# Performance work log

Hardware: AMD Instinct MI355X
Metric: run time of the kernel (lower is better)

## Reference

```python
import jax, jax.numpy as jnp
import numpy as np

PAD_IDX = 0
H = 500  # hidden_size hardcoded in the module
V = 50000
E = 500


def gru_scan(xs, h0, Wih, Whh, bih, bhh):
    """PyTorch-convention GRU over sequence. xs: (S, in), h0: (H,)."""
    def step(h, x):
        gi = x @ Wih.T + bih          # (3H,)
        gh = h @ Whh.T + bhh          # (3H,)
        ir, iz, inn = jnp.split(gi, 3)
        hr, hz, hn = jnp.split(gh, 3)
        r = jax.nn.sigmoid(ir + hr)
        z = jax.nn.sigmoid(iz + hz)
        n = jnp.tanh(inn + r * hn)
        h_new = (1.0 - z) * n + z * h
        return h_new, h_new
    h_last, hs = jax.lax.scan(step, h0, xs)
    return hs, h_last


def setup_inputs() -> dict:
    key = jax.random.key(0)
    ks = jax.random.split(key, 16)
    s = 0.05
    inp = {
        "encoder_input": jax.random.randint(ks[0], (512,), 0, V),
        "target_tensor": jax.random.randint(ks[1], (512,), 0, V),
        "encoder_hidden": jnp.zeros((1, 1, H), jnp.float32),
        # encoder params
        "enc_emb": jax.random.normal(ks[2], (V, E), jnp.float32) * s,
        "enc_Wih": jax.random.normal(ks[3], (3 * H, E), jnp.float32) * s,
        "enc_Whh": jax.random.normal(ks[4], (3 * H, H), jnp.float32) * s,
        "enc_bih": jax.random.normal(ks[5], (3 * H,), jnp.float32) * s,
        "enc_bhh": jax.random.normal(ks[6], (3 * H,), jnp.float32) * s,
        # decoder params
        "dec_emb": jax.random.normal(ks[7], (V, H), jnp.float32) * s,
        "dec_Wih": jax.random.normal(ks[8], (3 * H, H), jnp.float32) * s,
        "dec_Whh": jax.random.normal(ks[9], (3 * H, H), jnp.float32) * s,
        "dec_bih": jax.random.normal(ks[10], (3 * H,), jnp.float32) * s,
        "dec_bhh": jax.random.normal(ks[11], (3 * H,), jnp.float32) * s,
        "out_W": jax.random.normal(ks[12], (V, H), jnp.float32) * s,
        "out_b": jax.random.normal(ks[13], (V,), jnp.float32) * s,
    }
    return inp


def reference(encoder_input, target_tensor, encoder_hidden,
              enc_emb, enc_Wih, enc_Whh, enc_bih, enc_bhh,
              dec_emb, dec_Wih, dec_Whh, dec_bih, dec_bhh,
              out_W, out_b):
    # ---- Encoder: per-token GRU loop == one GRU scan over the sequence ----
    enc_x = enc_emb[encoder_input]                       # (S, E); dropout is identity (p=0 / eval)
    h0 = encoder_hidden[0, 0]                            # (H,)
    _, enc_h = gru_scan(enc_x, h0, enc_Wih, enc_Whh, enc_bih, enc_bhh)

    # ---- Decoder: teacher forcing; input di is target[di-1], first is PAD ----
    dec_in = jnp.concatenate([jnp.array([PAD_IDX], encoder_input.dtype),
                              target_tensor[:-1]])       # (T,)
    dec_x = jax.nn.relu(dec_emb[dec_in])                 # (T, H)
    dec_hs, _ = gru_scan(dec_x, enc_h, dec_Wih, dec_Whh, dec_bih, dec_bhh)  # (T, H)

    logits = dec_hs @ out_W.T + out_b                    # (T, V)
    logp = jax.nn.log_softmax(logits, axis=1)
    T = target_tensor.shape[0]
    # NLLLoss per step (batch=1 -> mean == single value), summed over steps
    loss = -jnp.sum(logp[jnp.arange(T), target_tensor])
    decoder_outputs = jnp.argmax(logp, axis=1).astype(jnp.int64)
    return loss, enc_h.reshape(1, 1, H), decoder_outputs
```

## Files before the change

kernel.cpp:

```cpp
#include <hip/hip_runtime.h>
#include <cstdint>
#include <cstddef>

#define H    500
#define G3   1500
#define SEQ  512
#define V    50000
#define NT   391

#define NB   25
#define HSL  20
#define ROWS 60

static constexpr size_t OFS_HBUF_E = 0;
static constexpr size_t OFS_HBUF_D = 16384;
static constexpr size_t OFS_ENCH   = 32768;
static constexpr size_t OFS_GI_ENC = 65536;
static constexpr size_t OFS_GI_DEC = OFS_GI_ENC + 3276800;
static constexpr size_t OFS_DECHS  = OFS_GI_DEC + 3276800;
static constexpr size_t OFS_SPART  = OFS_DECHS + 1048576;
static constexpr size_t OFS_PPART  = OFS_SPART + 1048576;
static constexpr size_t OFS_LTGT   = OFS_PPART + 2097152;
static constexpr size_t OFS_SFIN   = OFS_LTGT + 4096;

#define GI_BM 64
#define GI_BN 64
#define GI_BK 20
__global__ __launch_bounds__(256) void k_gi_gemm(
    const float* __restrict__ eA, const float* __restrict__ WA,
    const float* __restrict__ bA, const int* __restrict__ tA,
    const float* __restrict__ eB, const float* __restrict__ WB,
    const float* __restrict__ bB, const int* __restrict__ tB,
    float* __restrict__ GiA, float* __restrict__ GiB)
{
    const int dec = blockIdx.z;
    const float* emb = dec ? eB : eA;
    const float* Wih = dec ? WB : WA;
    const float* bih = dec ? bB : bA;
    const int*  toks = dec ? tB : tA;
    float* Gi        = dec ? GiB : GiA;

    __shared__ __align__(16) float As[GI_BK * GI_BM];
    __shared__ __align__(16) float Bs[GI_BK * GI_BN];
    const int tid = threadIdx.x;
    const int n0 = blockIdx.x * GI_BN;
    const int m0 = blockIdx.y * GI_BM;
    const int tx = tid & 15, ty = tid >> 4;
    float acc[4][4] = {};
    for (int k0 = 0; k0 < H; k0 += GI_BK) {
        for (int x = tid; x < 320; x += 256) {
            int m = x / 5, kq = x - m * 5;
            int gm = m0 + m;
            int tok = dec ? ((gm == 0) ? 0 : toks[gm - 1]) : toks[gm];
            float4 v = *(const float4*)(emb + (size_t)tok * H + k0 + kq * 4);
            if (dec) { v.x = fmaxf(v.x, 0.f); v.y = fmaxf(v.y, 0.f);
                       v.z = fmaxf(v.z, 0.f); v.w = fmaxf(v.w, 0.f); }
            int kb = kq * 4;
            As[(kb + 0) * GI_BM + m] = v.x; As[(kb + 1) * GI_BM + m] = v.y;
            As[(kb + 2) * GI_BM + m] = v.z; As[(kb + 3) * GI_BM + m] = v.w;
        }
        for (int x = tid; x < 320; x += 256) {
            int n = x / 5, kq = x - n * 5;
            int gn = n0 + n;
            float4 v = make_float4(0.f, 0.f, 0.f, 0.f);
            if (gn < G3) v = *(const float4*)(Wih + (size_t)gn * H + k0 + kq * 4);
            int kb = kq * 4;
            Bs[(kb + 0) * GI_BN + n] = v.x; Bs[(kb + 1) * GI_BN + n] = v.y;
            Bs[(kb + 2) * GI_BN + n] = v.z; Bs[(kb + 3) * GI_BN + n] = v.w;
        }
        __syncthreads();
#pragma unroll 5
        for (int kk = 0; kk < GI_BK; ++kk) {
            float a[4], b[4];
            *(float4*)&a[0] = *(const float4*)&As[kk * GI_BM + ty * 4];
            *(float4*)&b[0] = *(const float4*)&Bs[kk * GI_BN + tx * 4];
#pragma unroll
            for (int i = 0; i < 4; i++)
#pragma unroll
                for (int j = 0; j < 4; j++) acc[i][j] = fmaf(a[i], b[j], acc[i][j]);
        }
        __syncthreads();
    }
#pragma unroll
    for (int i = 0; i < 4; i++) {
        int gm = m0 + ty * 4 + i;
#pragma unroll
        for (int j = 0; j < 4; j++) {
            int gn = n0 + tx * 4 + j;
            if (gn < G3) Gi[(size_t)gm * G3 + gn] = acc[i][j] + bih[gn];
        }
    }
}

__global__ __launch_bounds__(256, 1) void k_gru(
    const float* __restrict__ Whh, const float* __restrict__ bhh,
    const float* __restrict__ Gi, const float* __restrict__ h0,
    unsigned long long* hbuf, float* hfinal, float* hs_out, float* douth, int S)
{
    __shared__ __align__(16) float h_s[H];
    __shared__ float p_s[ROWS * 26];
    __shared__ float gh_s[ROWS];
    const int tid = threadIdx.x;
    const int wg = blockIdx.x;
    const int j0 = wg * HSL;

    const int g = tid / 25;
    const int s = tid - g * 25;
    const int slc = tid / 10;
    const int e0  = 2 * (tid - slc * 10);

    float wreg[6][20];
    if (tid < 250) {
#pragma unroll
        for (int r = 0; r < 6; ++r) {
            const int rl = g * 6 + r;
            const int gate = rl / 20, jl = rl - gate * 20;
            const float* wr = Whh + (size_t)(gate * 500 + j0 + jl) * H + s * 20;
#pragma unroll
            for (int c = 0; c < 5; ++c)
                *(float4*)&wreg[r][c * 4] = *(const float4*)(wr + c * 4);
        }
    }
    float bb = 0.f;
    if (tid < ROWS) {
        const int gate = tid / 20, jl = tid - gate * 20;
        bb = bhh[gate * 500 + j0 + jl];
    }
    float hown = (tid < HSL) ? h0[j0 + tid] : 0.f;

    if (tid < HSL)
        __hip_atomic_store(hbuf + 800 + wg * 32 + tid,
                           ((unsigned long long)1u << 32) | (unsigned)__float_as_uint(hown),
                           __ATOMIC_RELAXED, __HIP_MEMORY_SCOPE_AGENT);

    for (int t = 0; t < S; ++t) {
        const unsigned want = (unsigned)(t + 1);
        const int rb = (t + 1) & 1;
        float ir = 0.f, iz = 0.f, inn = 0.f;
        if (tid < HSL) {
            const float* gi = Gi + (size_t)t * G3 + j0 + tid;
            ir = gi[0]; iz = gi[500]; inn = gi[1000];
        }
        if (tid < 250) {
            const unsigned long long* pa = hbuf + rb * 800 + slc * 32 + e0;
            unsigned long long v0, v1;
            do {
                v0 = __hip_atomic_load(pa,     __ATOMIC_RELAXED, __HIP_MEMORY_SCOPE_AGENT);
                v1 = __hip_atomic_load(pa + 1, __ATOMIC_RELAXED, __HIP_MEMORY_SCOPE_AGENT);
            } while (((unsigned)(v0 >> 32) != want) || ((unsigned)(v1 >> 32) != want));
            h_s[2 * tid]     = __uint_as_float((unsigned)v0);
            h_s[2 * tid + 1] = __uint_as_float((unsigned)v1);
        }
        __syncthreads();
        if (tid < 250) {
            float hv[20];
#pragma unroll
            for (int c = 0; c < 5; ++c)
                *(float4*)&hv[c * 4] = *(const float4*)&h_s[s * 20 + c * 4];
            float acc[6] = {0.f, 0.f, 0.f, 0.f, 0.f, 0.f};
#pragma unroll
            for (int i = 0; i < 20; ++i)
#pragma unroll
                for (int r = 0; r < 6; ++r) acc[r] = fmaf(wreg[r][i], hv[i], acc[r]);
#pragma unroll
            for (int r = 0; r < 6; ++r) p_s[(g * 6 + r) * 26 + s] = acc[r];
        }
        __syncthreads();
        if (tid < ROWS) {
            float sum = 0.f;
#pragma unroll 5
            for (int i = 0; i < 25; ++i) sum += p_s[tid * 26 + i];
            gh_s[tid] = sum + bb;
        }
        __syncthreads();
        if (tid < HSL) {
            const int j = j0 + tid;
            const float hr = gh_s[tid], hz = gh_s[HSL + tid], hn = gh_s[2 * HSL + tid];
            const float r = 1.f / (1.f + __expf(-(ir + hr)));
            const float z = 1.f / (1.f + __expf(-(iz + hz)));
            const float n = tanhf(inn + r * hn);
            const float hnew = (1.f - z) * n + z * hown;
            hown = hnew;
            __hip_atomic_store(hbuf + (t & 1) * 800 + wg * 32 + tid,
                               ((unsigned long long)(unsigned)(t + 2) << 32) |
                               (unsigned)__float_as_uint(hnew),
                               __ATOMIC_RELAXED, __HIP_MEMORY_SCOPE_AGENT);
            if (hs_out) hs_out[(size_t)t * H + j] = hnew;
            if (t == S - 1) {
                if (hfinal) hfinal[j] = hnew;
                if (douth)  douth[j]  = hnew;
            }
        }
    }
}

#define LG_BM 128
#define LG_BN 128
#define LG_BK 20
__global__ __launch_bounds__(256) void k_logits(
    const float* __restrict__ A, const float* __restrict__ Bw,
    const float* __restrict__ bias,
    float* __restrict__ S_part, unsigned long long* __restrict__ P_part)
{
    __shared__ __align__(16) float As[LG_BK * LG_BM];
    __shared__ __align__(16) float Bs[LG_BK * LG_BN];
    const int tid = threadIdx.x;
    const int bx = blockIdx.x;
    const int n0 = bx * LG_BN;
    const int m0 = blockIdx.y * LG_BM;
    const int tx = tid & 15, ty = tid >> 4;
    float acc[8][8] = {};
    for (int k0 = 0; k0 < H; k0 += LG_BK) {
        for (int x = tid; x < LG_BM * LG_BK; x += 256) {
            int m = x / LG_BK, k = x - m * LG_BK;
            As[k * LG_BM + m] = A[(size_t)(m0 + m) * H + k0 + k];
        }
        for (int x = tid; x < LG_BN * LG_BK; x += 256) {
            int n = x / LG_BK, k = x - n * LG_BK;
            int gn = n0 + n;
            Bs[k * LG_BN + n] = (gn < V) ? Bw[(size_t)gn * H + k0 + k] : 0.f;
        }
        __syncthreads();
#pragma unroll 5
        for (int kk = 0; kk < LG_BK; ++kk) {
            float a[8], b[8];
            *(float4*)&a[0] = *(const float4*)&As[kk * LG_BM + ty * 8];
            *(float4*)&a[4] = *(const float4*)&As[kk * LG_BM + ty * 8 + 4];
            *(float4*)&b[0] = *(const float4*)&Bs[kk * LG_BN + tx * 8];
            *(float4*)&b[4] = *(const float4*)&Bs[kk * LG_BN + tx * 8 + 4];
#pragma unroll
            for (int i = 0; i < 8; i++)
#pragma unroll
                for (int j = 0; j < 8; j++) acc[i][j] = fmaf(a[i], b[j], acc[i][j]);
        }
        __syncthreads();
    }
    float bcol[8]; int gncol[8]; bool bval[8];
#pragma unroll
    for (int j = 0; j < 8; j++) {
        int gn = n0 + tx * 8 + j;
        gncol[j] = gn; bval[j] = gn < V; bcol[j] = bval[j] ? bias[gn] : 0.f;
    }
#pragma unroll
    for (int i = 0; i < 8; i++) {
        int gm = m0 + ty * 8 + i;
        float mx = -3.4e38f; unsigned mi = 0; float se = 0.f;
#pragma unroll
        for (int j = 0; j < 8; j++) {
            if (bval[j]) {
                float l = acc[i][j] + bcol[j];
                se += __expf(l);
                if (l > mx) { mx = l; mi = (unsigned)gncol[j]; }
            }
        }
        unsigned u = __float_as_uint(mx);
        unsigned key = (u & 0x80000000u) ? ~u : (u | 0x80000000u);
        unsigned long long pk = ((unsigned long long)key << 32) |
                                (unsigned long long)(0xFFFFFFFFu - mi);
#pragma unroll
        for (int off = 1; off < 16; off <<= 1) {
            unsigned long long pk2 = __shfl_xor(pk, off);
            se += __shfl_xor(se, off);
            if (pk2 > pk) pk = pk2;
        }
        if (tx == 0) {
            S_part[(size_t)gm * NT + bx] = se;
            P_part[(size_t)gm * NT + bx] = pk;
        }
    }
}

__global__ __launch_bounds__(128) void k_reduce_rows(
    const float* __restrict__ S_part, const unsigned long long* __restrict__ P_part,
    float* __restrict__ Sfin, float* __restrict__ out_argmax)
{
    const int row = blockIdx.x, tid = threadIdx.x;
    float s = 0.f; unsigned long long p = 0ull;
    for (int i = tid; i < NT; i += 128) {
        s += S_part[(size_t)row * NT + i];
        unsigned long long q = P_part[(size_t)row * NT + i];
        if (q > p) p = q;
    }
#pragma unroll
    for (int off = 1; off < 64; off <<= 1) {
        s += __shfl_xor(s, off);
        unsigned long long q = __shfl_xor(p, off);
        if (q > p) p = q;
    }
    __shared__ float s2[2];
    __shared__ unsigned long long p2[2];
    if ((tid & 63) == 0) { s2[tid >> 6] = s; p2[tid >> 6] = p; }
    __syncthreads();
    if (tid == 0) {
        s = s2[0] + s2[1];
        p = p2[0] > p2[1] ? p2[0] : p2[1];
        Sfin[row] = s;
        unsigned idx = 0xFFFFFFFFu - (unsigned)(p & 0xFFFFFFFFull);
        out_argmax[row] = (float)idx;
    }
}

__global__ __launch_bounds__(64) void k_ltgt(
    const float* __restrict__ A, const float* __restrict__ Bw,
    const float* __restrict__ bias, const int* __restrict__ tgt,
    float* __restrict__ ltgt)
{
    const int row = blockIdx.x, lane = threadIdx.x;
    const int tok = tgt[row];
    const float* a = A + (size_t)row * H;
    const float* b = Bw + (size_t)tok * H;
    float s = 0.f;
    for (int k = lane; k < H; k += 64) s = fmaf(a[k], b[k], s);
#pragma unroll
    for (int off = 1; off < 64; off <<= 1) s += __shfl_xor(s, off);
    if (lane == 0) ltgt[row] = s + bias[tok];
}

__global__ __launch_bounds__(512) void k_final(
    const float* __restrict__ Sfin, const float* __restrict__ ltgt, float* __restrict__ d_out)
{
    __shared__ float red[512];
    const int t = threadIdx.x;
    red[t] = logf(Sfin[t]) - ltgt[t];
    __syncthreads();
    for (int s = 256; s > 0; s >>= 1) {
        if (t < s) red[t] += red[t + s];
        __syncthreads();
    }
    if (t == 0) d_out[0] = red[0];
}

extern "C" void kernel_launch(void* const* d_in, const int* in_sizes, int n_in,
                              void* d_out, int out_size, void* d_ws, size_t ws_size,
                              hipStream_t stream) {
    const int*   enc_ids = (const int*)d_in[0];
    const int*   tgt     = (const int*)d_in[1];
    const float* enc_h0  = (const float*)d_in[2];
    const float* enc_emb = (const float*)d_in[3];
    const float* enc_Wih = (const float*)d_in[4];
    const float* enc_Whh = (const float*)d_in[5];
    const float* enc_bih = (const float*)d_in[6];
    const float* enc_bhh = (const float*)d_in[7];
    const float* dec_emb = (const float*)d_in[8];
    const float* dec_Wih = (const float*)d_in[9];
    const float* dec_Whh = (const float*)d_in[10];
    const float* dec_bih = (const float*)d_in[11];
    const float* dec_bhh = (const float*)d_in[12];
    const float* out_W   = (const float*)d_in[13];
    const float* out_b   = (const float*)d_in[14];
    float* out = (float*)d_out;

    char* ws = (char*)d_ws;
    unsigned long long* hbufE = (unsigned long long*)(ws + OFS_HBUF_E);
    unsigned long long* hbufD = (unsigned long long*)(ws + OFS_HBUF_D);
    float* ench   = (float*)(ws + OFS_ENCH);
    float* gi_enc = (float*)(ws + OFS_GI_ENC);
    float* gi_dec = (float*)(ws + OFS_GI_DEC);
    float* dechs  = (float*)(ws + OFS_DECHS);
    float* Spart  = (float*)(ws + OFS_SPART);
    unsigned long long* Ppart = (unsigned long long*)(ws + OFS_PPART);
    float* ltgt   = (float*)(ws + OFS_LTGT);
    float* Sfin   = (float*)(ws + OFS_SFIN);

    k_gi_gemm<<<dim3(24, 8, 2), dim3(256), 0, stream>>>(
        enc_emb, enc_Wih, enc_bih, enc_ids,
        dec_emb, dec_Wih, dec_bih, tgt, gi_enc, gi_dec);
    k_gru<<<dim3(NB), dim3(256), 0, stream>>>(enc_Whh, enc_bhh, gi_enc, enc_h0,
                                              hbufE, ench, (float*)nullptr, out + 1, SEQ);
    k_gru<<<dim3(NB), dim3(256), 0, stream>>>(dec_Whh, dec_bhh, gi_dec, ench,
                                              hbufD, (float*)nullptr, dechs, (float*)nullptr, SEQ);
    k_ltgt<<<dim3(SEQ), dim3(64), 0, stream>>>(dechs, out_W, out_b, tgt, ltgt);
    k_logits<<<dim3(NT, 4), dim3(256), 0, stream>>>(dechs, out_W, out_b, Spart, Ppart);
    k_reduce_rows<<<dim3(SEQ), dim3(128), 0, stream>>>(Spart, Ppart, Sfin, out + 1 + H);
    k_final<<<dim3(1), dim3(512), 0, stream>>>(Sfin, ltgt, out);
}
```

Baseline: 2.563 ms.

## Fuse encoder and decoder GRU scans into one XCC-local persistent kernel

```diff
diff --git a/kernel.cpp b/kernel.cpp
--- a/kernel.cpp
+++ b/kernel.cpp
@@ -11,10 +11,10 @@
 #define NB   25
 #define HSL  20
 #define ROWS 60
+#define NWG_LAUNCH 256
 
 static constexpr size_t OFS_HBUF_E = 0;
-static constexpr size_t OFS_HBUF_D = 16384;
-static constexpr size_t OFS_ENCH   = 32768;
+static constexpr size_t OFS_CLAIM  = 32768;
 static constexpr size_t OFS_GI_ENC = 65536;
 static constexpr size_t OFS_GI_DEC = OFS_GI_ENC + 3276800;
 static constexpr size_t OFS_DECHS  = OFS_GI_DEC + 3276800;
@@ -22,6 +22,19 @@
 static constexpr size_t OFS_PPART  = OFS_SPART + 1048576;
 static constexpr size_t OFS_LTGT   = OFS_PPART + 2097152;
 static constexpr size_t OFS_SFIN   = OFS_LTGT + 4096;
+
+typedef unsigned int u32x4 __attribute__((ext_vector_type(4)));
+
+__device__ __forceinline__ u32x4 ld16_sc0(const unsigned long long* p) {
+    u32x4 r;
+    asm volatile("global_load_dwordx4 %0, %1, off sc0\n\ts_waitcnt vmcnt(0)"
+                 : "=v"(r) : "v"(p) : "memory");
+    return r;
+}
+__device__ __forceinline__ void st8_sc0(unsigned long long* p, unsigned long long v) {
+    asm volatile("global_store_dwordx2 %0, %1, off sc0"
+                 :: "v"(p), "v"(v) : "memory");
+}
 
 #define GI_BM 64
 #define GI_BN 64
@@ -31,8 +44,12 @@
     const float* __restrict__ bA, const int* __restrict__ tA,
     const float* __restrict__ eB, const float* __restrict__ WB,
     const float* __restrict__ bB, const int* __restrict__ tB,
-    float* __restrict__ GiA, float* __restrict__ GiB)
-{
+    float* __restrict__ GiA, float* __restrict__ GiB,
+    int* __restrict__ claim)
+{
+    if (blockIdx.x == 0 && blockIdx.y == 0 && blockIdx.z == 0 && threadIdx.x < 16)
+        claim[threadIdx.x] = (threadIdx.x == 8) ? -1 : 0;
+
     const int dec = blockIdx.z;
     const float* emb = dec ? eB : eA;
     const float* Wih = dec ? WB : WA;
@@ -92,22 +109,43 @@
     }
 }
 
-__global__ __launch_bounds__(256, 1) void k_gru(
-    const float* __restrict__ Whh, const float* __restrict__ bhh,
-    const float* __restrict__ Gi, const float* __restrict__ h0,
-    unsigned long long* hbuf, float* hfinal, float* hs_out, float* douth, int S)
+__global__ __launch_bounds__(256, 1) void k_gru2(
+    const float* __restrict__ eWhh, const float* __restrict__ ebhh,
+    const float* __restrict__ GiE,
+    const float* __restrict__ dWhh, const float* __restrict__ dbhh,
+    const float* __restrict__ GiD,
+    const float* __restrict__ h0, unsigned long long* hbuf, int* claim,
+    float* __restrict__ ench_out, float* __restrict__ dechs)
 {
     __shared__ __align__(16) float h_s[H];
     __shared__ float p_s[ROWS * 26];
     __shared__ float gh_s[ROWS];
+    __shared__ int wg_s;
     const int tid = threadIdx.x;
-    const int wg = blockIdx.x;
-    const int j0 = wg * HSL;
+
+    if (tid == 0) {
+        unsigned xcc;
+        asm volatile("s_getreg_b32 %0, hwreg(HW_REG_XCC_ID)" : "=s"(xcc));
+        int slot = -1;
+        int ticket = atomicAdd(claim + xcc, 1);
+        if (ticket < NB) {
+            if (ticket == NB - 1) atomicCAS(claim + 8, -1, (int)xcc);
+            int w;
+            do { w = __hip_atomic_load(claim + 8, __ATOMIC_RELAXED,
+                                       __HIP_MEMORY_SCOPE_AGENT); } while (w < 0);
+            if (w == (int)xcc) slot = ticket;
+        }
+        wg_s = slot;
+    }
+    __syncthreads();
+    const int wg = wg_s;
+    if (wg < 0) return;
 
     const int g = tid / 25;
     const int s = tid - g * 25;
     const int slc = tid / 10;
     const int e0  = 2 * (tid - slc * 10);
+    const int j0 = wg * HSL;
 
     float wreg[6][20];
     if (tid < 250) {
@@ -115,7 +153,7 @@
         for (int r = 0; r < 6; ++r) {
             const int rl = g * 6 + r;
             const int gate = rl / 20, jl = rl - gate * 20;
-            const float* wr = Whh + (size_t)(gate * 500 + j0 + jl) * H + s * 20;
+            const float* wr = eWhh + (size_t)(gate * 500 + j0 + jl) * H + s * 20;
 #pragma unroll
             for (int c = 0; c < 5; ++c)
                 *(float4*)&wreg[r][c * 4] = *(const float4*)(wr + c * 4);
@@ -124,32 +162,59 @@
     float bb = 0.f;
     if (tid < ROWS) {
         const int gate = tid / 20, jl = tid - gate * 20;
-        bb = bhh[gate * 500 + j0 + jl];
+        bb = ebhh[gate * 500 + j0 + jl];
     }
     float hown = (tid < HSL) ? h0[j0 + tid] : 0.f;
 
     if (tid < HSL)
-        __hip_atomic_store(hbuf + 800 + wg * 32 + tid,
-                           ((unsigned long long)1u << 32) | (unsigned)__float_as_uint(hown),
-                           __ATOMIC_RELAXED, __HIP_MEMORY_SCOPE_AGENT);
-
-    for (int t = 0; t < S; ++t) {
+        st8_sc0(hbuf + 800 + wg * 32 + tid,
+                ((unsigned long long)1u << 32) | (unsigned)__float_as_uint(hown));
+
+    for (int t = 0; t < 2 * SEQ; ++t) {
+        if (t == SEQ) {
+            if (tid < 250) {
+#pragma unroll
+                for (int r = 0; r < 6; ++r) {
+                    const int rl = g * 6 + r;
+                    const int gate = rl / 20, jl = rl - gate * 20;
+                    const float* wr = dWhh + (size_t)(gate * 500 + j0 + jl) * H + s * 20;
+#pragma unroll
+                    for (int c = 0; c < 5; ++c)
+                        *(float4*)&wreg[r][c * 4] = *(const float4*)(wr + c * 4);
+                }
+            }
+            if (tid < ROWS) {
+                const int gate = tid / 20, jl = tid - gate * 20;
+                bb = dbhh[gate * 500 + j0 + jl];
+            }
+        }
         const unsigned want = (unsigned)(t + 1);
         const int rb = (t + 1) & 1;
         float ir = 0.f, iz = 0.f, inn = 0.f;
         if (tid < HSL) {
-            const float* gi = Gi + (size_t)t * G3 + j0 + tid;
+            const float* gi = (t < SEQ ? GiE + (size_t)t * G3
+                                       : GiD + (size_t)(t - SEQ) * G3) + j0 + tid;
             ir = gi[0]; iz = gi[500]; inn = gi[1000];
         }
         if (tid < 250) {
             const unsigned long long* pa = hbuf + rb * 800 + slc * 32 + e0;
-            unsigned long long v0, v1;
-            do {
-                v0 = __hip_atomic_load(pa,     __ATOMIC_RELAXED, __HIP_MEMORY_SCOPE_AGENT);
-                v1 = __hip_atomic_load(pa + 1, __ATOMIC_RELAXED, __HIP_MEMORY_SCOPE_AGENT);
-            } while (((unsigned)(v0 >> 32) != want) || ((unsigned)(v1 >> 32) != want));
-            h_s[2 * tid]     = __uint_as_float((unsigned)v0);
-            h_s[2 * tid + 1] = __uint_as_float((unsigned)v1);
+            unsigned p0, p1;
+            int spin = 0;
+            for (;;) {
+                u32x4 v = ld16_sc0(pa);
+                if (v[1] == want && v[3] == want) { p0 = v[0]; p1 = v[2]; break; }
+                if (++spin > 48) {
+                    unsigned long long a = __hip_atomic_load(pa, __ATOMIC_RELAXED,
+                                                             __HIP_MEMORY_SCOPE_AGENT);
+                    unsigned long long b = __hip_atomic_load(pa + 1, __ATOMIC_RELAXED,
+                                                             __HIP_MEMORY_SCOPE_AGENT);
+                    if ((unsigned)(a >> 32) == want && (unsigned)(b >> 32) == want) {
+                        p0 = (unsigned)a; p1 = (unsigned)b; break;
+                    }
+                }
+            }
+            h_s[2 * tid]     = __uint_as_float(p0);
+            h_s[2 * tid + 1] = __uint_as_float(p1);
         }
         __syncthreads();
         if (tid < 250) {
@@ -181,15 +246,11 @@
             const float n = tanhf(inn + r * hn);
             const float hnew = (1.f - z) * n + z * hown;
             hown = hnew;
-            __hip_atomic_store(hbuf + (t & 1) * 800 + wg * 32 + tid,
-                               ((unsigned long long)(unsigned)(t + 2) << 32) |
-                               (unsigned)__float_as_uint(hnew),
-                               __ATOMIC_RELAXED, __HIP_MEMORY_SCOPE_AGENT);
-            if (hs_out) hs_out[(size_t)t * H + j] = hnew;
-            if (t == S - 1) {
-                if (hfinal) hfinal[j] = hnew;
-                if (douth)  douth[j]  = hnew;
-            }
+            st8_sc0(hbuf + (t & 1) * 800 + wg * 32 + tid,
+                    ((unsigned long long)(unsigned)(t + 2) << 32) |
+                    (unsigned)__float_as_uint(hnew));
+            if (t == SEQ - 1) ench_out[j] = hnew;
+            if (t >= SEQ) dechs[(size_t)(t - SEQ) * H + j] = hnew;
         }
     }
 }
@@ -352,8 +413,7 @@
 
     char* ws = (char*)d_ws;
     unsigned long long* hbufE = (unsigned long long*)(ws + OFS_HBUF_E);
-    unsigned long long* hbufD = (unsigned long long*)(ws + OFS_HBUF_D);
-    float* ench   = (float*)(ws + OFS_ENCH);
+    int*   claim  = (int*)(ws + OFS_CLAIM);
     float* gi_enc = (float*)(ws + OFS_GI_ENC);
     float* gi_dec = (float*)(ws + OFS_GI_DEC);
     float* dechs  = (float*)(ws + OFS_DECHS);
@@ -364,11 +424,10 @@
 
     k_gi_gemm<<<dim3(24, 8, 2), dim3(256), 0, stream>>>(
         enc_emb, enc_Wih, enc_bih, enc_ids,
-        dec_emb, dec_Wih, dec_bih, tgt, gi_enc, gi_dec);
-    k_gru<<<dim3(NB), dim3(256), 0, stream>>>(enc_Whh, enc_bhh, gi_enc, enc_h0,
-                                              hbufE, ench, (float*)nullptr, out + 1, SEQ);
-    k_gru<<<dim3(NB), dim3(256), 0, stream>>>(dec_Whh, dec_bhh, gi_dec, ench,
-                                              hbufD, (float*)nullptr, dechs, (float*)nullptr, SEQ);
+        dec_emb, dec_Wih, dec_bih, tgt, gi_enc, gi_dec, claim);
+    k_gru2<<<dim3(NWG_LAUNCH), dim3(256), 0, stream>>>(
+        enc_Whh, enc_bhh, gi_enc, dec_Whh, dec_bhh, gi_dec,
+        enc_h0, hbufE, claim, out + 1, dechs);
     k_ltgt<<<dim3(SEQ), dim3(64), 0, stream>>>(dechs, out_W, out_b, tgt, ltgt);
     k_logits<<<dim3(NT, 4), dim3(256), 0, stream>>>(dechs, out_W, out_b, Spart, Ppart);
     k_reduce_rows<<<dim3(SEQ), dim3(128), 0, stream>>>(Spart, Ppart, Sfin, out + 1 + H);
```

New measurement: 8.671 ms. 238% more time.

## Fuse decoder GRU with logits GEMM via ticketed persistent workers overlapping recurrence

Applied to the files above, without the earlier changes.

```diff
diff --git a/kernel.cpp b/kernel.cpp
--- a/kernel.cpp
+++ b/kernel.cpp
@@ -7,14 +7,17 @@
 #define SEQ  512
 #define V    50000
 #define NT   391
+#define NTILES (NT * 4)
 
 #define NB   25
 #define HSL  20
 #define ROWS 60
+#define NWORK 487
 
 static constexpr size_t OFS_HBUF_E = 0;
 static constexpr size_t OFS_HBUF_D = 16384;
 static constexpr size_t OFS_ENCH   = 32768;
+static constexpr size_t OFS_TICKET = 49152;
 static constexpr size_t OFS_GI_ENC = 65536;
 static constexpr size_t OFS_GI_DEC = OFS_GI_ENC + 3276800;
 static constexpr size_t OFS_DECHS  = OFS_GI_DEC + 3276800;
@@ -22,6 +25,15 @@
 static constexpr size_t OFS_PPART  = OFS_SPART + 1048576;
 static constexpr size_t OFS_LTGT   = OFS_PPART + 2097152;
 static constexpr size_t OFS_SFIN   = OFS_LTGT + 4096;
+
+__global__ __launch_bounds__(256) void k_init(unsigned long long* hbufE,
+                                              unsigned long long* hbufD,
+                                              int* ticket)
+{
+    const int tid = threadIdx.x;
+    for (int i = tid; i < 1600; i += 256) { hbufE[i] = 0ull; hbufD[i] = 0ull; }
+    if (tid == 0) *ticket = 0;
+}
 
 #define GI_BM 64
 #define GI_BN 64
@@ -95,7 +107,7 @@
 __global__ __launch_bounds__(256, 1) void k_gru(
     const float* __restrict__ Whh, const float* __restrict__ bhh,
     const float* __restrict__ Gi, const float* __restrict__ h0,
-    unsigned long long* hbuf, float* hfinal, float* hs_out, float* douth, int S)
+    unsigned long long* hbuf, float* hfinal, float* douth, int S)
 {
     __shared__ __align__(16) float h_s[H];
     __shared__ float p_s[ROWS * 26];
@@ -185,7 +197,6 @@
                                ((unsigned long long)(unsigned)(t + 2) << 32) |
                                (unsigned)__float_as_uint(hnew),
                                __ATOMIC_RELAXED, __HIP_MEMORY_SCOPE_AGENT);
-            if (hs_out) hs_out[(size_t)t * H + j] = hnew;
             if (t == S - 1) {
                 if (hfinal) hfinal[j] = hnew;
                 if (douth)  douth[j]  = hnew;
@@ -197,75 +208,220 @@
 #define LG_BM 128
 #define LG_BN 128
 #define LG_BK 20
-__global__ __launch_bounds__(256) void k_logits(
-    const float* __restrict__ A, const float* __restrict__ Bw,
-    const float* __restrict__ bias,
-    float* __restrict__ S_part, unsigned long long* __restrict__ P_part)
-{
+__global__ __launch_bounds__(256, 1) void k_dec_fused(
+    const float* __restrict__ Whh, const float* __restrict__ bhh,
+    const float* __restrict__ Gi,  const float* __restrict__ h0,
+    unsigned long long* hbuf, float* __restrict__ dechs,
+    const float* __restrict__ outW, const float* __restrict__ outb,
+    float* __restrict__ S_part, unsigned long long* __restrict__ P_part,
+    int* ticket)
+{
+    const int tid = threadIdx.x;
+
+    if (blockIdx.x < NB) {
+        __builtin_amdgcn_s_setprio(2);
+        __shared__ __align__(16) float h_s[H];
+        __shared__ float p_s[ROWS * 26];
+        __shared__ float gh_s[ROWS];
+        const int wg = blockIdx.x;
+        const int j0 = wg * HSL;
+        const int g = tid / 25;
+        const int s = tid - g * 25;
+        const int slc = tid / 10;
+        const int e0  = 2 * (tid - slc * 10);
+
+        float wreg[6][20];
+        if (tid < 250) {
+#pragma unroll
+            for (int r = 0; r < 6; ++r) {
+                const int rl = g * 6 + r;
+                const int gate = rl / 20, jl = rl - gate * 20;
+                const float* wr = Whh + (size_t)(gate * 500 + j0 + jl) * H + s * 20;
+#pragma unroll
+                for (int c = 0; c < 5; ++c)
+                    *(float4*)&wreg[r][c * 4] = *(const float4*)(wr + c * 4);
+            }
+        }
+        float bb = 0.f;
+        if (tid < ROWS) {
+            const int gate = tid / 20, jl = tid - gate * 20;
+            bb = bhh[gate * 500 + j0 + jl];
+        }
+        float hown = (tid < HSL) ? h0[j0 + tid] : 0.f;
+
+        if (tid < HSL)
+            __hip_atomic_store(hbuf + 800 + wg * 32 + tid,
+                               ((unsigned long long)1u << 32) | (unsigned)__float_as_uint(hown),
+                               __ATOMIC_RELAXED, __HIP_MEMORY_SCOPE_AGENT);
+
+        for (int t = 0; t < SEQ; ++t) {
+            const unsigned want = (unsigned)(t + 1);
+            const int rb = (t + 1) & 1;
+            float ir = 0.f, iz = 0.f, inn = 0.f;
+            if (tid < HSL) {
+                const float* gi = Gi + (size_t)t * G3 + j0 + tid;
+                ir = gi[0]; iz = gi[500]; inn = gi[1000];
+            }
+            if (tid < 250) {
+                const unsigned long long* pa = hbuf + rb * 800 + slc * 32 + e0;
+                unsigned long long v0, v1;
+                do {
+                    v0 = __hip_atomic_load(pa,     __ATOMIC_RELAXED, __HIP_MEMORY_SCOPE_AGENT);
+                    v1 = __hip_atomic_load(pa + 1, __ATOMIC_RELAXED, __HIP_MEMORY_SCOPE_AGENT);
+                } while (((unsigned)(v0 >> 32) != want) || ((unsigned)(v1 >> 32) != want));
+                h_s[2 * tid]     = __uint_as_float((unsigned)v0);
+                h_s[2 * tid + 1] = __uint_as_float((unsigned)v1);
+            }
+            __syncthreads();
+            if (tid < 250) {
+                float hv[20];
+#pragma unroll
+                for (int c = 0; c < 5; ++c)
+                    *(float4*)&hv[c * 4] = *(const float4*)&h_s[s * 20 + c * 4];
+                float acc[6] = {0.f, 0.f, 0.f, 0.f, 0.f, 0.f};
+#pragma unroll
+                for (int i = 0; i < 20; ++i)
+#pragma unroll
+                    for (int r = 0; r < 6; ++r) acc[r] = fmaf(wreg[r][i], hv[i], acc[r]);
+#pragma unroll
+                for (int r = 0; r < 6; ++r) p_s[(g * 6 + r) * 26 + s] = acc[r];
+            }
+            __syncthreads();
+            if (tid < ROWS) {
+                float sum = 0.f;
+#pragma unroll 5
+                for (int i = 0; i < 25; ++i) sum += p_s[tid * 26 + i];
+                gh_s[tid] = sum + bb;
+            }
+            __syncthreads();
+            if (tid < HSL) {
+                const int j = j0 + tid;
+                const float hr = gh_s[tid], hz = gh_s[HSL + tid], hn = gh_s[2 * HSL + tid];
+                const float r = 1.f / (1.f + __expf(-(ir + hr)));
+                const float z = 1.f / (1.f + __expf(-(iz + hz)));
+                const float n = tanhf(inn + r * hn);
+                const float hnew = (1.f - z) * n + z * hown;
+                hown = hnew;
+                __hip_atomic_store(&dechs[(size_t)t * H + j], hnew,
+                                   __ATOMIC_RELAXED, __HIP_MEMORY_SCOPE_AGENT);
+                const unsigned long long w =
+                    ((unsigned long long)(unsigned)(t + 2) << 32) |
+                    (unsigned)__float_as_uint(hnew);
+                if ((t & 127) == 127)
+                    __hip_atomic_store(hbuf + (t & 1) * 800 + wg * 32 + tid, w,
+                                       __ATOMIC_RELEASE, __HIP_MEMORY_SCOPE_AGENT);
+                else
+                    __hip_atomic_store(hbuf + (t & 1) * 800 + wg * 32 + tid, w,
+                                       __ATOMIC_RELAXED, __HIP_MEMORY_SCOPE_AGENT);
+            }
+        }
+        return;
+    }
+
     __shared__ __align__(16) float As[LG_BK * LG_BM];
     __shared__ __align__(16) float Bs[LG_BK * LG_BN];
-    const int tid = threadIdx.x;
-    const int bx = blockIdx.x;
-    const int n0 = bx * LG_BN;
-    const int m0 = blockIdx.y * LG_BM;
-    const int tx = tid & 15, ty = tid >> 4;
-    float acc[8][8] = {};
-    for (int k0 = 0; k0 < H; k0 += LG_BK) {
-        for (int x = tid; x < LG_BM * LG_BK; x += 256) {
-            int m = x / LG_BK, k = x - m * LG_BK;
-            As[k * LG_BM + m] = A[(size_t)(m0 + m) * H + k0 + k];
-        }
-        for (int x = tid; x < LG_BN * LG_BK; x += 256) {
-            int n = x / LG_BK, k = x - n * LG_BK;
-            int gn = n0 + n;
-            Bs[k * LG_BN + n] = (gn < V) ? Bw[(size_t)gn * H + k0 + k] : 0.f;
-        }
-        __syncthreads();
+    __shared__ int go;
+
+    for (;;) {
+        __syncthreads();
+        if (tid == 0) go = atomicAdd(ticket, 1);
+        __syncthreads();
+        const int tk = go;
+        if (tk >= NTILES) return;
+        const int by = tk / NT, bx = tk - by * NT;
+        const int n0 = bx * LG_BN;
+        const int m0 = by * LG_BM;
+
+        const unsigned T_need = (unsigned)(m0 + 129);
+        if (tid < 64) {
+            for (;;) {
+                unsigned mn = 0xFFFFFFFFu;
+                for (int i = tid; i < 500; i += 64) {
+                    const int sl = i / 20, j = i - sl * 20;
+                    unsigned long long w = __hip_atomic_load(
+                        hbuf + 800 + sl * 32 + j,
+                        __ATOMIC_RELAXED, __HIP_MEMORY_SCOPE_AGENT);
+                    unsigned tg = (unsigned)(w >> 32);
+                    mn = mn < tg ? mn : tg;
+                }
+#pragma unroll
+                for (int off = 32; off; off >>= 1) {
+                    unsigned o = __shfl_xor(mn, off);
+                    mn = mn < o ? mn : o;
+                }
+                if (mn >= T_need) break;
+                __builtin_amdgcn_s_sleep(32);
+            }
+        }
+        __syncthreads();
+        __threadfence();
+
+        const int tx = tid & 15, ty = tid >> 4;
+        float acc[8][8] = {};
+        for (int k0 = 0; k0 < H; k0 += LG_BK) {
+            for (int x = tid; x < 640; x += 256) {
+                int m = x / 5, kq = x - m * 5;
+                float4 v = *(const float4*)(dechs + (size_t)(m0 + m) * H + k0 + kq * 4);
+                int kb = kq * 4;
+                As[(kb + 0) * LG_BM + m] = v.x; As[(kb + 1) * LG_BM + m] = v.y;
+                As[(kb + 2) * LG_BM + m] = v.z; As[(kb + 3) * LG_BM + m] = v.w;
+            }
+            for (int x = tid; x < 640; x += 256) {
+                int n = x / 5, kq = x - n * 5;
+                int gn = n0 + n;
+                float4 v = make_float4(0.f, 0.f, 0.f, 0.f);
+                if (gn < V) v = *(const float4*)(outW + (size_t)gn * H + k0 + kq * 4);
+                int kb = kq * 4;
+                Bs[(kb + 0) * LG_BN + n] = v.x; Bs[(kb + 1) * LG_BN + n] = v.y;
+                Bs[(kb + 2) * LG_BN + n] = v.z; Bs[(kb + 3) * LG_BN + n] = v.w;
+            }
+            __syncthreads();
 #pragma unroll 5
-        for (int kk = 0; kk < LG_BK; ++kk) {
-            float a[8], b[8];
-            *(float4*)&a[0] = *(const float4*)&As[kk * LG_BM + ty * 8];
-            *(float4*)&a[4] = *(const float4*)&As[kk * LG_BM + ty * 8 + 4];
-            *(float4*)&b[0] = *(const float4*)&Bs[kk * LG_BN + tx * 8];
-            *(float4*)&b[4] = *(const float4*)&Bs[kk * LG_BN + tx * 8 + 4];
-#pragma unroll
-            for (int i = 0; i < 8; i++)
-#pragma unroll
-                for (int j = 0; j < 8; j++) acc[i][j] = fmaf(a[i], b[j], acc[i][j]);
-        }
-        __syncthreads();
-    }
-    float bcol[8]; int gncol[8]; bool bval[8];
-#pragma unroll
-    for (int j = 0; j < 8; j++) {
-        int gn = n0 + tx * 8 + j;
-        gncol[j] = gn; bval[j] = gn < V; bcol[j] = bval[j] ? bias[gn] : 0.f;
-    }
-#pragma unroll
-    for (int i = 0; i < 8; i++) {
-        int gm = m0 + ty * 8 + i;
-        float mx = -3.4e38f; unsigned mi = 0; float se = 0.f;
+            for (int kk = 0; kk < LG_BK; ++kk) {
+                float a[8], b[8];
+                *(float4*)&a[0] = *(const float4*)&As[kk * LG_BM + ty * 8];
+                *(float4*)&a[4] = *(const float4*)&As[kk * LG_BM + ty * 8 + 4];
+                *(float4*)&b[0] = *(const float4*)&Bs[kk * LG_BN + tx * 8];
+                *(float4*)&b[4] = *(const float4*)&Bs[kk * LG_BN + tx * 8 + 4];
+#pragma unroll
+                for (int i = 0; i < 8; i++)
+#pragma unroll
+                    for (int j = 0; j < 8; j++) acc[i][j] = fmaf(a[i], b[j], acc[i][j]);
+            }
+            __syncthreads();
+        }
+        float bcol[8]; int gncol[8]; bool bval[8];
 #pragma unroll
         for (int j = 0; j < 8; j++) {
-            if (bval[j]) {
-                float l = acc[i][j] + bcol[j];
-                se += __expf(l);
-                if (l > mx) { mx = l; mi = (unsigned)gncol[j]; }
-            }
-        }
-        unsigned u = __float_as_uint(mx);
-        unsigned key = (u & 0x80000000u) ? ~u : (u | 0x80000000u);
-        unsigned long long pk = ((unsigned long long)key << 32) |
-                                (unsigned long long)(0xFFFFFFFFu - mi);
-#pragma unroll
-        for (int off = 1; off < 16; off <<= 1) {
-            unsigned long long pk2 = __shfl_xor(pk, off);
-            se += __shfl_xor(se, off);
-            if (pk2 > pk) pk = pk2;
-        }
-        if (tx == 0) {
-            S_part[(size_t)gm * NT + bx] = se;
-            P_part[(size_t)gm * NT + bx] = pk;
+            int gn = n0 + tx * 8 + j;
+            gncol[j] = gn; bval[j] = gn < V; bcol[j] = bval[j] ? outb[gn] : 0.f;
+        }
+#pragma unroll
+        for (int i = 0; i < 8; i++) {
+            int gm = m0 + ty * 8 + i;
+            float mx = -3.4e38f; unsigned mi = 0; float se = 0.f;
+#pragma unroll
+            for (int j = 0; j < 8; j++) {
+                if (bval[j]) {
+                    float l = acc[i][j] + bcol[j];
+                    se += __expf(l);
+                    if (l > mx) { mx = l; mi = (unsigned)gncol[j]; }
+                }
+            }
+            unsigned u = __float_as_uint(mx);
+            unsigned key = (u & 0x80000000u) ? ~u : (u | 0x80000000u);
+            unsigned long long pk = ((unsigned long long)key << 32) |
+                                    (unsigned long long)(0xFFFFFFFFu - mi);
+#pragma unroll
+            for (int off = 1; off < 16; off <<= 1) {
+                unsigned long long pk2 = __shfl_xor(pk, off);
+                se += __shfl_xor(se, off);
+                if (pk2 > pk) pk = pk2;
+            }
+            if (tx == 0) {
+                S_part[(size_t)gm * NT + bx] = se;
+                P_part[(size_t)gm * NT + bx] = pk;
+            }
         }
     }
 }
@@ -354,6 +510,7 @@
     unsigned long long* hbufE = (unsigned long long*)(ws + OFS_HBUF_E);
     unsigned long long* hbufD = (unsigned long long*)(ws + OFS_HBUF_D);
     float* ench   = (float*)(ws + OFS_ENCH);
+    int*   ticket = (int*)(ws + OFS_TICKET);
     float* gi_enc = (float*)(ws + OFS_GI_ENC);
     float* gi_dec = (float*)(ws + OFS_GI_DEC);
     float* dechs  = (float*)(ws + OFS_DECHS);
@@ -362,15 +519,16 @@
     float* ltgt   = (float*)(ws + OFS_LTGT);
     float* Sfin   = (float*)(ws + OFS_SFIN);
 
+    k_init<<<dim3(1), dim3(256), 0, stream>>>(hbufE, hbufD, ticket);
     k_gi_gemm<<<dim3(24, 8, 2), dim3(256), 0, stream>>>(
         enc_emb, enc_Wih, enc_bih, enc_ids,
         dec_emb, dec_Wih, dec_bih, tgt, gi_enc, gi_dec);
     k_gru<<<dim3(NB), dim3(256), 0, stream>>>(enc_Whh, enc_bhh, gi_enc, enc_h0,
-                                              hbufE, ench, (float*)nullptr, out + 1, SEQ);
-    k_gru<<<dim3(NB), dim3(256), 0, stream>>>(dec_Whh, dec_bhh, gi_dec, ench,
-                                              hbufD, (float*)nullptr, dechs, (float*)nullptr, SEQ);
+                                              hbufE, ench, out + 1, SEQ);
+    k_dec_fused<<<dim3(NB + NWORK), dim3(256), 0, stream>>>(
+        dec_Whh, dec_bhh, gi_dec, ench, hbufD, dechs,
+        out_W, out_b, Spart, Ppart, ticket);
     k_ltgt<<<dim3(SEQ), dim3(64), 0, stream>>>(dechs, out_W, out_b, tgt, ltgt);
-    k_logits<<<dim3(NT, 4), dim3(256), 0, stream>>>(dechs, out_W, out_b, Spart, Ppart);
     k_reduce_rows<<<dim3(SEQ), dim3(128), 0, stream>>>(Spart, Ppart, Sfin, out + 1 + H);
     k_final<<<dim3(1), dim3(512), 0, stream>>>(Sfin, ltgt, out);
 }
```

Measured after the change: 2.337 ms. 8.8% less time.
